# Kernel optimization log

Measured on AMD Instinct MI355X. Metric: run time of the kernel, lower is better.

Reference implementation:

```python
import jax, jax.numpy as jnp
import numpy as np

D_MODEL = 1024
NUM_HEADS = 16
HEAD_DIM = D_MODEL // NUM_HEADS

def _trunc_normal(key, shape, std):
    # truncated normal in [-3*std, 3*std]
    return jax.random.truncated_normal(key, -3.0, 3.0, shape, dtype=jnp.float32) * std

def setup_inputs() -> dict:
    key = jax.random.key(0)
    kx, kq, kk, kv, ko = jax.random.split(key, 5)
    std = np.sqrt(2.0 / (D_MODEL + D_MODEL))
    return {
        "in_features": jax.random.normal(kx, (4, 2048, D_MODEL), dtype=jnp.float32),
        "weight_q": _trunc_normal(kq, (D_MODEL, D_MODEL), std),
        "weight_k": _trunc_normal(kk, (D_MODEL, D_MODEL), std),
        "weight_v": _trunc_normal(kv, (D_MODEL, D_MODEL), std),
        "weight_o": _trunc_normal(ko, (D_MODEL, D_MODEL), std),
    }

def reference(in_features, weight_q, weight_k, weight_v, weight_o):
    in_dtype = in_features.dtype
    x = in_features.astype(jnp.float32)
    B, S, _ = x.shape
    # projections: x @ W.T (matches torch matmul(x, weight.T))
    Q = x @ weight_q.T
    K = x @ weight_k.T
    V = x @ weight_v.T
    # [B, H, S, hd]
    Q = Q.reshape(B, S, NUM_HEADS, HEAD_DIM).transpose(0, 2, 1, 3)
    K = K.reshape(B, S, NUM_HEADS, HEAD_DIM).transpose(0, 2, 1, 3)
    V = V.reshape(B, S, NUM_HEADS, HEAD_DIM).transpose(0, 2, 1, 3)
    scores = jnp.einsum('bhqd,bhkd->bhqk', Q, K) / jnp.sqrt(jnp.float32(HEAD_DIM))
    causal = jnp.tril(jnp.ones((S, S), dtype=bool))  # [S, S]
    scores = jnp.where(causal, scores, -jnp.inf)
    attn = jax.nn.softmax(scores, axis=-1)
    out = jnp.einsum('bhqk,bhkd->bhqd', attn, V)  # [B, H, S, hd]
    out = out.transpose(0, 2, 1, 3).reshape(B, S, D_MODEL)
    out = out @ weight_o.T
    return out.astype(in_dtype)
```

## Files before the change

kernel.cpp:

```cpp
#include <hip/hip_runtime.h>
#include <stdint.h>
#include <math.h>

#define B_SZ 4
#define S_LEN 2048
#define NH 16
#define HD 64
#define DM 1024
#define M_ROWS (B_SZ * S_LEN)
#define NQ 16

typedef __bf16 bf16x8 __attribute__((ext_vector_type(8)));
typedef __bf16 bf16x4 __attribute__((ext_vector_type(4)));
typedef float f32x4 __attribute__((ext_vector_type(4)));
typedef unsigned int u32x2 __attribute__((ext_vector_type(2)));

typedef __attribute__((address_space(3))) void lds_t;
typedef __attribute__((address_space(1))) const void gbl_t;

__device__ __forceinline__ unsigned cvtpk_bf16(float a, float b) {
  unsigned r;
  asm("v_cvt_pk_bf16_f32 %0, %1, %2" : "=v"(r) : "v"(a), "v"(b));
  return r;
}

__global__ void cvt_f32_bf16(const float* __restrict__ in,
                             __bf16* __restrict__ out, int n4) {
  int i = blockIdx.x * blockDim.x + threadIdx.x;
  int stride = gridDim.x * blockDim.x;
  for (; i < n4; i += stride) {
    f32x4 v = reinterpret_cast<const f32x4*>(in)[i];
    bf16x4 o;
    o[0] = (__bf16)v[0]; o[1] = (__bf16)v[1];
    o[2] = (__bf16)v[2]; o[3] = (__bf16)v[3];
    reinterpret_cast<bf16x4*>(out)[i] = o;
  }
}

__global__ void cvt_weights(const float* __restrict__ wq, const float* __restrict__ wk,
                            const float* __restrict__ wv, const float* __restrict__ wo,
                            __bf16* __restrict__ dst) {
  const int N4 = DM * DM / 4;
  int i = blockIdx.x * blockDim.x + threadIdx.x;
  int stride = gridDim.x * blockDim.x;
  for (; i < 4 * N4; i += stride) {
    int sel = i >> 18;
    const float* src = (sel == 0) ? wq : (sel == 1) ? wk : (sel == 2) ? wv : wo;
    f32x4 v = reinterpret_cast<const f32x4*>(src)[i & (N4 - 1)];
    bf16x4 o;
    o[0] = (__bf16)v[0]; o[1] = (__bf16)v[1];
    o[2] = (__bf16)v[2]; o[3] = (__bf16)v[3];
    reinterpret_cast<bf16x4*>(dst)[i] = o;
  }
}

template <int MODE>
__global__ __launch_bounds__(256, 2) void gemm64(
    const unsigned short* __restrict__ A, const unsigned short* __restrict__ BT,
    __bf16* __restrict__ Qb, __bf16* __restrict__ Kb, __bf16* __restrict__ Vt,
    float* __restrict__ Out, int NX) {
  __shared__ __align__(16) unsigned short As[128 * 64];
  __shared__ __align__(16) unsigned short Bs[128 * 64];

  const int t = threadIdx.x, lane = t & 63, w = t >> 6;
  const int wm = w >> 1, wn = w & 1;
  const int g = lane >> 4, c = lane & 15;

  const int nwg = (int)gridDim.x;
  const int cpx = nwg >> 3;
  const int bid = (int)blockIdx.x;
  const int wg = (bid & 7) * cpx + (bid >> 3);
  const int bx = wg % NX, by = wg / NX;
  const int tm0 = by * 128, tn0 = bx * 128;
  const int K = DM;

  const int srow = t >> 3;
  const int scolb = (t & 7) << 4;
  const int ssw = scolb ^ ((srow & 7) << 4);
  const uint8_t* gA0 = (const uint8_t*)A + ((size_t)(tm0 + srow) * K) * 2 + ssw;
  const uint8_t* gB0 = (const uint8_t*)BT + ((size_t)(tn0 + srow) * K) * 2 + ssw;
  uint8_t* lA0 = (uint8_t*)As + t * 16;
  uint8_t* lB0 = (uint8_t*)Bs + t * 16;
  const int kxor = (c & 7) << 4;

  f32x4 acc[4][4] = {};

  for (int k0 = 0; k0 < K; k0 += 64) {
#pragma unroll
    for (int q = 0; q < 4; ++q) {
      __builtin_amdgcn_global_load_lds((gbl_t*)(gA0 + ((size_t)q * 32 * K + k0) * 2),
                                       (lds_t*)(lA0 + q * 4096), 16, 0, 0);
      __builtin_amdgcn_global_load_lds((gbl_t*)(gB0 + ((size_t)q * 32 * K + k0) * 2),
                                       (lds_t*)(lB0 + q * 4096), 16, 0, 0);
    }
    __syncthreads();

#pragma unroll
    for (int ks = 0; ks < 2; ++ks) {
      bf16x8 af[4], bfm[4];
#pragma unroll
      for (int mb = 0; mb < 4; ++mb)
        af[mb] = *reinterpret_cast<const bf16x8*>(
            (const uint8_t*)As + (wm * 64 + mb * 16 + c) * 128 + ((ks * 64 + g * 16) ^ kxor));
#pragma unroll
      for (int nb = 0; nb < 4; ++nb)
        bfm[nb] = *reinterpret_cast<const bf16x8*>(
            (const uint8_t*)Bs + (wn * 64 + nb * 16 + c) * 128 + ((ks * 64 + g * 16) ^ kxor));
#pragma unroll
      for (int mb = 0; mb < 4; ++mb)
#pragma unroll
        for (int nb = 0; nb < 4; ++nb)
          acc[mb][nb] = __builtin_amdgcn_mfma_f32_16x16x32_bf16(af[mb], bfm[nb], acc[mb][nb], 0, 0, 0);
    }
    __syncthreads();
  }

  const int rm0 = tm0 + wm * 64;
  const int cn0 = tn0 + wn * 64;
  const int sel = tn0 >> 10;
#pragma unroll
  for (int mb = 0; mb < 4; ++mb) {
#pragma unroll
    for (int nb = 0; nb < 4; ++nb) {
      f32x4 v = acc[mb][nb];
#pragma unroll
      for (int j = 0; j < 4; ++j) {
        int rm = rm0 + mb * 16 + g * 4 + j;
        int cn = cn0 + nb * 16 + c;
        float val = v[j];
        if (MODE == 0) {
          int b = rm >> 11, s = rm & 2047;
          int dmn = cn & 1023;
          int h = dmn >> 6, d = dmn & 63;
          if (sel == 0) {
            Qb[(((size_t)(b * NH + h) * S_LEN + s) << 6) + d] = (__bf16)(val * 0.125f);
          } else if (sel == 1) {
            Kb[(((size_t)(b * NH + h) * S_LEN + s) << 6) + d] = (__bf16)val;
          } else {
            Vt[((size_t)(b * NH + h) * HD + d) * S_LEN + s] = (__bf16)val;
          }
        } else {
          Out[(size_t)rm * DM + cn] = val;
        }
      }
    }
  }
}

template <int SPLIT>
__global__ __launch_bounds__(256, 3) void attn_kernel(
    const unsigned short* __restrict__ Qb, const unsigned short* __restrict__ Kb,
    const unsigned short* __restrict__ Vt, __bf16* __restrict__ Aout,
    __bf16* __restrict__ AP, float* __restrict__ Lp) {
  __shared__ __align__(16) unsigned short KVs[2][8192];
  __shared__ __align__(16) unsigned short Ps[4][32 * 72];

  const int t = threadIdx.x, lane = t & 63, w = t >> 6;
  const int g = lane >> 4, c = lane & 15;
  const int bh = blockIdx.y;
  const int qx = (NQ - 1) - (int)blockIdx.x / SPLIT;
  const int sp = (int)blockIdx.x % SPLIT;
  const int b = bh >> 4, h = bh & 15;
  const int q0 = qx * 128 + w * 32;

  const unsigned short* Qp = Qb + (size_t)bh * S_LEN * HD;
  const uint8_t* Kg8 = (const uint8_t*)(Kb + (size_t)bh * S_LEN * HD);
  const uint8_t* Vg8 = (const uint8_t*)(Vt + (size_t)bh * HD * S_LEN);

  const int sr = t >> 3;
  const int scb = ((t & 7) << 4) ^ ((sr & 7) << 4);
  const uint8_t* Kst = Kg8 + (size_t)sr * 128 + scb;
  const uint8_t* Vst = Vg8 + (size_t)sr * (S_LEN * 2) + scb;
  uint8_t* Ls = (uint8_t*)&KVs[0][0];

#define STAGE(buf, kvb_) do {                                                  \
    uint8_t* kd = Ls + (buf) * 16384 + t * 16;                                 \
    const uint8_t* kg = Kst + (size_t)(kvb_) * 128;                            \
    const uint8_t* vg = Vst + (size_t)(kvb_) * 2;                              \
    __builtin_amdgcn_global_load_lds((gbl_t*)kg, (lds_t*)kd, 16, 0, 0);        \
    __builtin_amdgcn_global_load_lds((gbl_t*)(kg + 32 * 128),                  \
                                     (lds_t*)(kd + 4096), 16, 0, 0);           \
    __builtin_amdgcn_global_load_lds((gbl_t*)vg, (lds_t*)(kd + 8192), 16, 0, 0);\
    __builtin_amdgcn_global_load_lds((gbl_t*)(vg + (size_t)32 * S_LEN * 2),    \
                                     (lds_t*)(kd + 12288), 16, 0, 0);          \
  } while (0)

  bf16x8 qf[2][2];
#pragma unroll
  for (int mb = 0; mb < 2; ++mb)
#pragma unroll
    for (int ks = 0; ks < 2; ++ks)
      qf[mb][ks] = *reinterpret_cast<const bf16x8*>(
          Qp + (size_t)(q0 + mb * 16 + c) * HD + ks * 32 + g * 8);

  bf16x8 onesf;
#pragma unroll
  for (int i = 0; i < 8; ++i) onesf[i] = (__bf16)1.0f;

  f32x4 oacc[2][4] = {};
  f32x4 lacc[2] = {};

  const int kxor = (c & 7) << 4;
  const int n_total = 2 * qx + 2;
  const int chunk = (n_total + SPLIT - 1) / SPLIT;
  int t0 = sp * chunk; if (t0 > n_total) t0 = n_total;
  int t1 = t0 + chunk; if (t1 > n_total) t1 = n_total;
  const int nblk_w = (q0 >> 6) + 1;

  const int st0 = (t0 < n_total) ? t0 : (n_total - 1);
  STAGE(0, st0 * 64);
  __syncthreads();

  __bf16* psw = (__bf16*)&Ps[w][0];
  const int qr = q0 + c;

  for (int kb = t0; kb < t1; ++kb) {
    const int cur = (kb - t0) & 1;
    if (kb + 1 < t1) STAGE(cur ^ 1, (kb + 1) * 64);

    if (kb < nblk_w) {
      const int kvb = kb * 64;
      const uint8_t* KL = Ls + cur * 16384;
      const uint8_t* VL = KL + 8192;

      f32x4 sacc[2][4] = {};
      __builtin_amdgcn_s_setprio(1);
#pragma unroll
      for (int ks = 0; ks < 2; ++ks) {
#pragma unroll
        for (int nb = 0; nb < 4; ++nb) {
          bf16x8 kf = *reinterpret_cast<const bf16x8*>(
              KL + (nb * 16 + c) * 128 + ((ks * 64 + g * 16) ^ kxor));
          sacc[0][nb] = __builtin_amdgcn_mfma_f32_16x16x32_bf16(kf, qf[0][ks], sacc[0][nb], 0, 0, 0);
          sacc[1][nb] = __builtin_amdgcn_mfma_f32_16x16x32_bf16(kf, qf[1][ks], sacc[1][nb], 0, 0, 0);
        }
      }
      __builtin_amdgcn_s_setprio(0);

      if (kb == nblk_w - 1) {
#pragma unroll
        for (int mb = 0; mb < 2; ++mb) {
          const int qrm = qr + mb * 16;
#pragma unroll
          for (int nb = 0; nb < 4; ++nb) {
            const int key0 = kvb + nb * 16 + g * 4;
            float p0 = (key0 + 0 <= qrm) ? __expf(sacc[mb][nb][0]) : 0.f;
            float p1 = (key0 + 1 <= qrm) ? __expf(sacc[mb][nb][1]) : 0.f;
            float p2 = (key0 + 2 <= qrm) ? __expf(sacc[mb][nb][2]) : 0.f;
            float p3 = (key0 + 3 <= qrm) ? __expf(sacc[mb][nb][3]) : 0.f;
            u32x2 pk = {cvtpk_bf16(p0, p1), cvtpk_bf16(p2, p3)};
            *reinterpret_cast<u32x2*>(psw + (mb * 16 + c) * 72 + nb * 16 + g * 4) = pk;
          }
        }
      } else {
#pragma unroll
        for (int mb = 0; mb < 2; ++mb)
#pragma unroll
          for (int nb = 0; nb < 4; ++nb) {
            float p0 = __expf(sacc[mb][nb][0]);
            float p1 = __expf(sacc[mb][nb][1]);
            float p2 = __expf(sacc[mb][nb][2]);
            float p3 = __expf(sacc[mb][nb][3]);
            u32x2 pk = {cvtpk_bf16(p0, p1), cvtpk_bf16(p2, p3)};
            *reinterpret_cast<u32x2*>(psw + (mb * 16 + c) * 72 + nb * 16 + g * 4) = pk;
          }
      }

      bf16x8 pf0_0 = *reinterpret_cast<const bf16x8*>(psw + (c) * 72 + g * 8);
      bf16x8 pf0_1 = *reinterpret_cast<const bf16x8*>(psw + (c) * 72 + 32 + g * 8);
      bf16x8 pf1_0 = *reinterpret_cast<const bf16x8*>(psw + (16 + c) * 72 + g * 8);
      bf16x8 pf1_1 = *reinterpret_cast<const bf16x8*>(psw + (16 + c) * 72 + 32 + g * 8);

      __builtin_amdgcn_s_setprio(1);
      lacc[0] = __builtin_amdgcn_mfma_f32_16x16x32_bf16(pf0_0, onesf, lacc[0], 0, 0, 0);
      lacc[0] = __builtin_amdgcn_mfma_f32_16x16x32_bf16(pf0_1, onesf, lacc[0], 0, 0, 0);
      lacc[1] = __builtin_amdgcn_mfma_f32_16x16x32_bf16(pf1_0, onesf, lacc[1], 0, 0, 0);
      lacc[1] = __builtin_amdgcn_mfma_f32_16x16x32_bf16(pf1_1, onesf, lacc[1], 0, 0, 0);

#pragma unroll
      for (int db = 0; db < 4; ++db) {
        bf16x8 vf0 = *reinterpret_cast<const bf16x8*>(
            VL + (db * 16 + c) * 128 + ((g * 16) ^ kxor));
        bf16x8 vf1 = *reinterpret_cast<const bf16x8*>(
            VL + (db * 16 + c) * 128 + ((64 + g * 16) ^ kxor));
        oacc[0][db] = __builtin_amdgcn_mfma_f32_16x16x32_bf16(pf0_0, vf0, oacc[0][db], 0, 0, 0);
        oacc[0][db] = __builtin_amdgcn_mfma_f32_16x16x32_bf16(pf0_1, vf1, oacc[0][db], 0, 0, 0);
        oacc[1][db] = __builtin_amdgcn_mfma_f32_16x16x32_bf16(pf1_0, vf0, oacc[1][db], 0, 0, 0);
        oacc[1][db] = __builtin_amdgcn_mfma_f32_16x16x32_bf16(pf1_1, vf1, oacc[1][db], 0, 0, 0);
      }
      __builtin_amdgcn_s_setprio(0);
    }
    __syncthreads();
  }
#undef STAGE

  if (SPLIT == 1) {
    float rl[2][4];
#pragma unroll
    for (int mb = 0; mb < 2; ++mb)
#pragma unroll
      for (int j = 0; j < 4; ++j) rl[mb][j] = 1.0f / lacc[mb][j];
#pragma unroll
    for (int mb = 0; mb < 2; ++mb)
#pragma unroll
      for (int db = 0; db < 4; ++db)
#pragma unroll
        for (int j = 0; j < 4; ++j) {
          float o = oacc[mb][db][j] * rl[mb][j];
          int s = q0 + mb * 16 + g * 4 + j;
          int d = db * 16 + c;
          Aout[(size_t)(b * S_LEN + s) * DM + h * HD + d] = (__bf16)o;
        }
  } else {
    __bf16* APs = AP + (size_t)(sp * (B_SZ * NH) + bh) * S_LEN * HD;
    float* Lps = Lp + (size_t)(sp * (B_SZ * NH) + bh) * S_LEN;
#pragma unroll
    for (int mb = 0; mb < 2; ++mb) {
#pragma unroll
      for (int db = 0; db < 4; ++db)
#pragma unroll
        for (int j = 0; j < 4; ++j) {
          int q = q0 + mb * 16 + g * 4 + j;
          APs[(size_t)q * HD + db * 16 + c] = (__bf16)oacc[mb][db][j];
        }
      if (c == 0) {
#pragma unroll
        for (int j = 0; j < 4; ++j)
          Lps[q0 + mb * 16 + g * 4 + j] = lacc[mb][j];
      }
    }
  }
}

__global__ void attn_combine4(const __bf16* __restrict__ AP, const float* __restrict__ Lp,
                              __bf16* __restrict__ Aout) {
  const int NIT = B_SZ * NH * S_LEN * (HD / 8);
  int i = blockIdx.x * blockDim.x + threadIdx.x;
  int stride = gridDim.x * blockDim.x;
  const size_t SOFF = (size_t)(B_SZ * NH) * S_LEN * HD;
  const size_t LOFF = (size_t)(B_SZ * NH) * S_LEN;
  for (; i < NIT; i += stride) {
    int d8 = i & 7;
    int q = (i >> 3) & (S_LEN - 1);
    int bh = i >> 14;
    size_t base = ((size_t)bh * S_LEN + q) * HD + d8 * 8;
    size_t lbase = (size_t)bh * S_LEN + q;
    float l = Lp[lbase] + Lp[LOFF + lbase] + Lp[2 * LOFF + lbase] + Lp[3 * LOFF + lbase];
    float rl = 1.0f / l;
    bf16x8 a0 = *reinterpret_cast<const bf16x8*>(AP + base);
    bf16x8 a1 = *reinterpret_cast<const bf16x8*>(AP + SOFF + base);
    bf16x8 a2 = *reinterpret_cast<const bf16x8*>(AP + 2 * SOFF + base);
    bf16x8 a3 = *reinterpret_cast<const bf16x8*>(AP + 3 * SOFF + base);
    int b = bh >> 4, h = bh & 15;
    bf16x8 o;
#pragma unroll
    for (int k = 0; k < 8; ++k)
      o[k] = (__bf16)((((float)a0[k] + (float)a1[k]) + ((float)a2[k] + (float)a3[k])) * rl);
    *reinterpret_cast<bf16x8*>(Aout + ((size_t)(b * S_LEN + q)) * DM + h * HD + d8 * 8) = o;
  }
}

extern "C" void kernel_launch(void* const* d_in, const int* in_sizes, int n_in,
                              void* d_out, int out_size, void* d_ws, size_t ws_size,
                              hipStream_t stream) {
  const float* x = (const float*)d_in[0];
  const float* wq = (const float*)d_in[1];
  const float* wk = (const float*)d_in[2];
  const float* wv = (const float*)d_in[3];
  const float* wo = (const float*)d_in[4];
  float* out = (float*)d_out;

  uint8_t* ws = (uint8_t*)d_ws;
  const size_t MB = 1024 * 1024;
  unsigned short* xb   = (unsigned short*)(ws);
  unsigned short* wcat = (unsigned short*)(ws + 16 * MB);
  unsigned short* wob  = (unsigned short*)(ws + 22 * MB);
  unsigned short* Qb   = (unsigned short*)(ws + 24 * MB);
  unsigned short* Kb   = (unsigned short*)(ws + 40 * MB);
  unsigned short* Vt   = (unsigned short*)(ws + 56 * MB);
  __bf16* AP           = (__bf16*)(ws + 72 * MB);
  float* Lp            = (float*)(ws + 16 * MB);

  {
    int n4x = (M_ROWS * DM) / 4;
    int blk = (n4x + 255) / 256; if (blk > 2048) blk = 2048;
    cvt_f32_bf16<<<blk, 256, 0, stream>>>(x, (__bf16*)xb, n4x);
    cvt_weights<<<1024, 256, 0, stream>>>(wq, wk, wv, wo, (__bf16*)wcat);
  }

  gemm64<0><<<dim3((3 * DM / 128) * (M_ROWS / 128)), 256, 0, stream>>>(
      xb, wcat, (__bf16*)Qb, (__bf16*)Kb, (__bf16*)Vt, nullptr, 3 * DM / 128);

  __bf16* Aout = (__bf16*)xb;
  if (ws_size >= (size_t)136 * MB) {
    attn_kernel<4><<<dim3(NQ * 4, B_SZ * NH), 256, 0, stream>>>(
        Qb, Kb, Vt, Aout, AP, Lp);
    attn_combine4<<<2048, 256, 0, stream>>>(AP, Lp, Aout);
  } else {
    attn_kernel<1><<<dim3(NQ, B_SZ * NH), 256, 0, stream>>>(
        Qb, Kb, Vt, Aout, nullptr, nullptr);
  }

  gemm64<1><<<dim3((DM / 128) * (M_ROWS / 128)), 256, 0, stream>>>(
      xb, wob, nullptr, nullptr, nullptr, out, DM / 128);
}
```

Baseline: 204.5 us.

## Use 256x128 tile QKV GEMM with 8 waves and phased prefetch pipeline

```diff
diff --git a/kernel.cpp b/kernel.cpp
--- a/kernel.cpp
+++ b/kernel.cpp
@@ -54,17 +54,144 @@
   }
 }
 
-template <int MODE>
-__global__ __launch_bounds__(256, 2) void gemm64(
+__global__ __launch_bounds__(512, 2) void gemm256_qkv(
     const unsigned short* __restrict__ A, const unsigned short* __restrict__ BT,
-    __bf16* __restrict__ Qb, __bf16* __restrict__ Kb, __bf16* __restrict__ Vt,
-    float* __restrict__ Out, int NX) {
+    __bf16* __restrict__ Qb, __bf16* __restrict__ Kb, __bf16* __restrict__ Vt) {
+  __shared__ __align__(16) uint8_t L[2][49152];
+
+  const int t = threadIdx.x, lane = t & 63;
+  const int wid = t >> 6;
+  const int wm = wid >> 1, wn = wid & 1;
+  const int g = lane >> 4, c = lane & 15;
+
+  const int bid = (int)blockIdx.x;
+  const int wg = (bid & 7) * 96 + (bid >> 3);
+  const int bx = wg % 24, by = wg / 24;
+  const int tm0 = by * 256, tn0 = bx * 128;
+  const int K = DM;
+
+  const int u0 = t >> 3;
+  const int colswz = ((t & 7) << 4) ^ ((u0 & 7) << 4);
+  const uint8_t* Ag = (const uint8_t*)A;
+  const uint8_t* Bg = (const uint8_t*)BT;
+
+  const int arow0 = (u0 >> 5) * 64 + (u0 & 31);
+#define STAGE_A(buf_, h_, kb_) do {                                            \
+    const uint8_t* s0 = Ag + ((size_t)(tm0 + arow0 + (h_) * 32) * K) * 2 +     \
+                        (kb_) * 128 + colswz;                                  \
+    uint8_t* d = &L[buf_][0] + (h_) * 16384 + t * 16;                          \
+    __builtin_amdgcn_global_load_lds((gbl_t*)s0, (lds_t*)d, 16, 0, 0);         \
+    __builtin_amdgcn_global_load_lds((gbl_t*)(s0 + (size_t)128 * K * 2),       \
+                                     (lds_t*)(d + 8192), 16, 0, 0);            \
+  } while (0)
+#define STAGE_B(buf_, h_, kb_) do {                                            \
+    const uint8_t* s0 = Bg + ((size_t)(tn0 + arow0 + (h_) * 32) * K) * 2 +     \
+                        (kb_) * 128 + colswz;                                  \
+    uint8_t* d = &L[buf_][0] + 32768 + (h_) * 8192 + t * 16;                   \
+    __builtin_amdgcn_global_load_lds((gbl_t*)s0, (lds_t*)d, 16, 0, 0);         \
+  } while (0)
+
+  const int kxor = (c & 7) << 4;
+  f32x4 acc[4][4] = {};
+
+  STAGE_A(0, 0, 0); STAGE_A(0, 1, 0);
+  STAGE_B(0, 0, 0); STAGE_B(0, 1, 0);
+  asm volatile("s_waitcnt vmcnt(0)" ::: "memory");
+  asm volatile("s_barrier" ::: "memory");
+
+#define PHASE(buf_, MH, NH, WAITSTR, ISSUE) do {                               \
+    const uint8_t* Ab = &L[buf_][0];                                           \
+    const uint8_t* Bb = &L[buf_][0] + 32768;                                   \
+    bf16x8 af[2][2], bf[2][2];                                                 \
+    _Pragma("unroll") for (int i = 0; i < 2; ++i) {                            \
+      const int mf = MH * 2 + i;                                               \
+      const int r = (mf >> 1) * 16384 + (wm * 32 + (mf & 1) * 16 + c) * 128;   \
+      af[i][0] = *reinterpret_cast<const bf16x8*>(Ab + r + ((g * 16) ^ kxor)); \
+      af[i][1] = *reinterpret_cast<const bf16x8*>(Ab + r + ((64 + g * 16) ^ kxor)); \
+    }                                                                          \
+    _Pragma("unroll") for (int j = 0; j < 2; ++j) {                            \
+      const int nf = NH * 2 + j;                                               \
+      const int r = (nf >> 1) * 8192 + (wn * 32 + (nf & 1) * 16 + c) * 128;    \
+      bf[j][0] = *reinterpret_cast<const bf16x8*>(Bb + r + ((g * 16) ^ kxor)); \
+      bf[j][1] = *reinterpret_cast<const bf16x8*>(Bb + r + ((64 + g * 16) ^ kxor)); \
+    }                                                                          \
+    WAITSTR;                                                                   \
+    ISSUE;                                                                     \
+    asm volatile("s_barrier" ::: "memory");                                    \
+    __builtin_amdgcn_s_setprio(1);                                            \
+    _Pragma("unroll") for (int i = 0; i < 2; ++i)                              \
+      _Pragma("unroll") for (int j = 0; j < 2; ++j) {                          \
+        acc[MH * 2 + i][NH * 2 + j] = __builtin_amdgcn_mfma_f32_16x16x32_bf16( \
+            af[i][0], bf[j][0], acc[MH * 2 + i][NH * 2 + j], 0, 0, 0);         \
+        acc[MH * 2 + i][NH * 2 + j] = __builtin_amdgcn_mfma_f32_16x16x32_bf16( \
+            af[i][1], bf[j][1], acc[MH * 2 + i][NH * 2 + j], 0, 0, 0);         \
+      }                                                                        \
+    __builtin_amdgcn_s_setprio(0);                                            \
+    asm volatile("s_barrier" ::: "memory");                                    \
+  } while (0)
+
+  const int NT = K / 64;
+  for (int kb = 0; kb < NT; ++kb) {
+    const int cur = kb & 1;
+    const int nxt = cur ^ 1;
+    const int kn = (kb + 1 < NT) ? (kb + 1) : (NT - 1);
+    const int kc = kn * 128;
+
+    PHASE(cur, 0, 0,
+          asm volatile("s_waitcnt vmcnt(2)" ::: "memory"),
+          STAGE_A(nxt, 0, kn));
+    PHASE(cur, 0, 1,
+          asm volatile("s_waitcnt vmcnt(2)" ::: "memory"),
+          do { STAGE_B(nxt, 0, kn); STAGE_B(nxt, 1, kn); } while (0));
+    PHASE(cur, 1, 0, (void)0, STAGE_A(nxt, 1, kn));
+    PHASE(cur, 1, 1,
+          asm volatile("s_waitcnt vmcnt(3)" ::: "memory"),
+          (void)0);
+    (void)kc;
+  }
+  asm volatile("s_waitcnt vmcnt(0)" ::: "memory");
+#undef PHASE
+#undef STAGE_A
+#undef STAGE_B
+
+  const int rm0 = tm0 + wm * 64;
+  const int cn0 = tn0 + wn * 64;
+  const int sel = tn0 >> 10;
+#pragma unroll
+  for (int mf = 0; mf < 4; ++mf) {
+#pragma unroll
+    for (int nf = 0; nf < 4; ++nf) {
+      f32x4 v = acc[mf][nf];
+#pragma unroll
+      for (int j = 0; j < 4; ++j) {
+        int rm = rm0 + mf * 16 + g * 4 + j;
+        int cn = cn0 + nf * 16 + c;
+        int b = rm >> 11, s = rm & 2047;
+        int dmn = cn & 1023;
+        int h = dmn >> 6, d = dmn & 63;
+        float val = v[j];
+        if (sel == 0) {
+          Qb[(((size_t)(b * NH + h) * S_LEN + s) << 6) + d] = (__bf16)(val * 0.125f);
+        } else if (sel == 1) {
+          Kb[(((size_t)(b * NH + h) * S_LEN + s) << 6) + d] = (__bf16)val;
+        } else {
+          Vt[((size_t)(b * NH + h) * HD + d) * S_LEN + s] = (__bf16)val;
+        }
+      }
+    }
+  }
+}
+
+__global__ __launch_bounds__(256, 2) void gemm64_o(
+    const unsigned short* __restrict__ A, const unsigned short* __restrict__ BT,
+    float* __restrict__ Out) {
   __shared__ __align__(16) unsigned short As[128 * 64];
   __shared__ __align__(16) unsigned short Bs[128 * 64];
 
   const int t = threadIdx.x, lane = t & 63, w = t >> 6;
   const int wm = w >> 1, wn = w & 1;
   const int g = lane >> 4, c = lane & 15;
+  const int NX = DM / 128;
 
   const int nwg = (int)gridDim.x;
   const int cpx = nwg >> 3;
@@ -117,9 +244,8 @@
 
   const int rm0 = tm0 + wm * 64;
   const int cn0 = tn0 + wn * 64;
-  const int sel = tn0 >> 10;
-#pragma unroll
-  for (int mb = 0; mb < 4; ++mb) {
+#pragma unroll
+  for (int mb = 0; mb < 4; ++mb)
 #pragma unroll
     for (int nb = 0; nb < 4; ++nb) {
       f32x4 v = acc[mb][nb];
@@ -127,24 +253,9 @@
       for (int j = 0; j < 4; ++j) {
         int rm = rm0 + mb * 16 + g * 4 + j;
         int cn = cn0 + nb * 16 + c;
-        float val = v[j];
-        if (MODE == 0) {
-          int b = rm >> 11, s = rm & 2047;
-          int dmn = cn & 1023;
-          int h = dmn >> 6, d = dmn & 63;
-          if (sel == 0) {
-            Qb[(((size_t)(b * NH + h) * S_LEN + s) << 6) + d] = (__bf16)(val * 0.125f);
-          } else if (sel == 1) {
-            Kb[(((size_t)(b * NH + h) * S_LEN + s) << 6) + d] = (__bf16)val;
-          } else {
-            Vt[((size_t)(b * NH + h) * HD + d) * S_LEN + s] = (__bf16)val;
-          }
-        } else {
-          Out[(size_t)rm * DM + cn] = val;
-        }
+        Out[(size_t)rm * DM + cn] = v[j];
       }
     }
-  }
 }
 
 template <int SPLIT>
@@ -388,8 +499,8 @@
     cvt_weights<<<1024, 256, 0, stream>>>(wq, wk, wv, wo, (__bf16*)wcat);
   }
 
-  gemm64<0><<<dim3((3 * DM / 128) * (M_ROWS / 128)), 256, 0, stream>>>(
-      xb, wcat, (__bf16*)Qb, (__bf16*)Kb, (__bf16*)Vt, nullptr, 3 * DM / 128);
+  gemm256_qkv<<<dim3(768), 512, 0, stream>>>(
+      xb, wcat, (__bf16*)Qb, (__bf16*)Kb, (__bf16*)Vt);
 
   __bf16* Aout = (__bf16*)xb;
   if (ws_size >= (size_t)136 * MB) {
@@ -401,6 +512,5 @@
         Qb, Kb, Vt, Aout, nullptr, nullptr);
   }
 
-  gemm64<1><<<dim3((DM / 128) * (M_ROWS / 128)), 256, 0, stream>>>(
-      xb, wob, nullptr, nullptr, nullptr, out, DM / 128);
-}
+  gemm64_o<<<dim3((DM / 128) * (M_ROWS / 128)), 256, 0, stream>>>(xb, wob, out);
+}
```

Result: slower. 210.8 us (+3.1%).

## Double-buffer GEMM LDS tiles, raise MFMA priority, merge conversion kernels

Applied to the files above, without the earlier changes.

```diff
diff --git a/kernel.cpp b/kernel.cpp
--- a/kernel.cpp
+++ b/kernel.cpp
@@ -24,33 +24,33 @@
   return r;
 }
 
-__global__ void cvt_f32_bf16(const float* __restrict__ in,
-                             __bf16* __restrict__ out, int n4) {
+__global__ void cvt_all(const float* __restrict__ x,
+                        const float* __restrict__ wq, const float* __restrict__ wk,
+                        const float* __restrict__ wv, const float* __restrict__ wo,
+                        __bf16* __restrict__ xb, __bf16* __restrict__ wdst) {
+  const int NX4 = M_ROWS * DM / 4;
+  const int NW4 = DM * DM / 4;
+  const int TOT = NX4 + 4 * NW4;
   int i = blockIdx.x * blockDim.x + threadIdx.x;
   int stride = gridDim.x * blockDim.x;
-  for (; i < n4; i += stride) {
-    f32x4 v = reinterpret_cast<const f32x4*>(in)[i];
+  for (; i < TOT; i += stride) {
+    const float* src;
+    __bf16* dst;
+    int idx;
+    if (i < NX4) {
+      src = x; dst = xb; idx = i;
+    } else {
+      int j = i - NX4;
+      int sel = j >> 18;
+      src = (sel == 0) ? wq : (sel == 1) ? wk : (sel == 2) ? wv : wo;
+      dst = wdst + (size_t)sel * DM * DM;
+      idx = j & (NW4 - 1);
+    }
+    f32x4 v = reinterpret_cast<const f32x4*>(src)[idx];
     bf16x4 o;
     o[0] = (__bf16)v[0]; o[1] = (__bf16)v[1];
     o[2] = (__bf16)v[2]; o[3] = (__bf16)v[3];
-    reinterpret_cast<bf16x4*>(out)[i] = o;
-  }
-}
-
-__global__ void cvt_weights(const float* __restrict__ wq, const float* __restrict__ wk,
-                            const float* __restrict__ wv, const float* __restrict__ wo,
-                            __bf16* __restrict__ dst) {
-  const int N4 = DM * DM / 4;
-  int i = blockIdx.x * blockDim.x + threadIdx.x;
-  int stride = gridDim.x * blockDim.x;
-  for (; i < 4 * N4; i += stride) {
-    int sel = i >> 18;
-    const float* src = (sel == 0) ? wq : (sel == 1) ? wk : (sel == 2) ? wv : wo;
-    f32x4 v = reinterpret_cast<const f32x4*>(src)[i & (N4 - 1)];
-    bf16x4 o;
-    o[0] = (__bf16)v[0]; o[1] = (__bf16)v[1];
-    o[2] = (__bf16)v[2]; o[3] = (__bf16)v[3];
-    reinterpret_cast<bf16x4*>(dst)[i] = o;
+    reinterpret_cast<bf16x4*>(dst)[idx] = o;
   }
 }
 
@@ -59,8 +59,8 @@
     const unsigned short* __restrict__ A, const unsigned short* __restrict__ BT,
     __bf16* __restrict__ Qb, __bf16* __restrict__ Kb, __bf16* __restrict__ Vt,
     float* __restrict__ Out, int NX) {
-  __shared__ __align__(16) unsigned short As[128 * 64];
-  __shared__ __align__(16) unsigned short Bs[128 * 64];
+  __shared__ __align__(16) unsigned short As[2][128 * 64];
+  __shared__ __align__(16) unsigned short Bs[2][128 * 64];
 
   const int t = threadIdx.x, lane = t & 63, w = t >> 6;
   const int wm = w >> 1, wn = w & 1;
@@ -79,41 +79,53 @@
   const int ssw = scolb ^ ((srow & 7) << 4);
   const uint8_t* gA0 = (const uint8_t*)A + ((size_t)(tm0 + srow) * K) * 2 + ssw;
   const uint8_t* gB0 = (const uint8_t*)BT + ((size_t)(tn0 + srow) * K) * 2 + ssw;
-  uint8_t* lA0 = (uint8_t*)As + t * 16;
-  uint8_t* lB0 = (uint8_t*)Bs + t * 16;
   const int kxor = (c & 7) << 4;
 
+#define STAGE(buf_, k0_) do {                                                  \
+    uint8_t* lA = (uint8_t*)&As[buf_][0] + t * 16;                             \
+    uint8_t* lB = (uint8_t*)&Bs[buf_][0] + t * 16;                             \
+    _Pragma("unroll") for (int q = 0; q < 4; ++q) {                            \
+      __builtin_amdgcn_global_load_lds(                                        \
+          (gbl_t*)(gA0 + ((size_t)q * 32 * K + (k0_)) * 2),                    \
+          (lds_t*)(lA + q * 4096), 16, 0, 0);                                  \
+      __builtin_amdgcn_global_load_lds(                                        \
+          (gbl_t*)(gB0 + ((size_t)q * 32 * K + (k0_)) * 2),                    \
+          (lds_t*)(lB + q * 4096), 16, 0, 0);                                  \
+    }                                                                          \
+  } while (0)
+
   f32x4 acc[4][4] = {};
 
-  for (int k0 = 0; k0 < K; k0 += 64) {
-#pragma unroll
-    for (int q = 0; q < 4; ++q) {
-      __builtin_amdgcn_global_load_lds((gbl_t*)(gA0 + ((size_t)q * 32 * K + k0) * 2),
-                                       (lds_t*)(lA0 + q * 4096), 16, 0, 0);
-      __builtin_amdgcn_global_load_lds((gbl_t*)(gB0 + ((size_t)q * 32 * K + k0) * 2),
-                                       (lds_t*)(lB0 + q * 4096), 16, 0, 0);
+  STAGE(0, 0);
+  __syncthreads();
+
+  const int NT = K / 64;
+  for (int kt = 0; kt < NT; ++kt) {
+    const int cur = kt & 1;
+    if (kt + 1 < NT) STAGE(cur ^ 1, (kt + 1) * 64);
+
+#pragma unroll
+    for (int ks = 0; ks < 2; ++ks) {
+      bf16x8 af[4], bfm[4];
+#pragma unroll
+      for (int mb = 0; mb < 4; ++mb)
+        af[mb] = *reinterpret_cast<const bf16x8*>(
+            (const uint8_t*)&As[cur][0] + (wm * 64 + mb * 16 + c) * 128 + ((ks * 64 + g * 16) ^ kxor));
+#pragma unroll
+      for (int nb = 0; nb < 4; ++nb)
+        bfm[nb] = *reinterpret_cast<const bf16x8*>(
+            (const uint8_t*)&Bs[cur][0] + (wn * 64 + nb * 16 + c) * 128 + ((ks * 64 + g * 16) ^ kxor));
+      __builtin_amdgcn_s_setprio(1);
+#pragma unroll
+      for (int mb = 0; mb < 4; ++mb)
+#pragma unroll
+        for (int nb = 0; nb < 4; ++nb)
+          acc[mb][nb] = __builtin_amdgcn_mfma_f32_16x16x32_bf16(af[mb], bfm[nb], acc[mb][nb], 0, 0, 0);
+      __builtin_amdgcn_s_setprio(0);
     }
     __syncthreads();
-
-#pragma unroll
-    for (int ks = 0; ks < 2; ++ks) {
-      bf16x8 af[4], bfm[4];
-#pragma unroll
-      for (int mb = 0; mb < 4; ++mb)
-        af[mb] = *reinterpret_cast<const bf16x8*>(
-            (const uint8_t*)As + (wm * 64 + mb * 16 + c) * 128 + ((ks * 64 + g * 16) ^ kxor));
-#pragma unroll
-      for (int nb = 0; nb < 4; ++nb)
-        bfm[nb] = *reinterpret_cast<const bf16x8*>(
-            (const uint8_t*)Bs + (wn * 64 + nb * 16 + c) * 128 + ((ks * 64 + g * 16) ^ kxor));
-#pragma unroll
-      for (int mb = 0; mb < 4; ++mb)
-#pragma unroll
-        for (int nb = 0; nb < 4; ++nb)
-          acc[mb][nb] = __builtin_amdgcn_mfma_f32_16x16x32_bf16(af[mb], bfm[nb], acc[mb][nb], 0, 0, 0);
-    }
-    __syncthreads();
-  }
+  }
+#undef STAGE
 
   const int rm0 = tm0 + wm * 64;
   const int cn0 = tn0 + wn * 64;
@@ -381,12 +393,7 @@
   __bf16* AP           = (__bf16*)(ws + 72 * MB);
   float* Lp            = (float*)(ws + 16 * MB);
 
-  {
-    int n4x = (M_ROWS * DM) / 4;
-    int blk = (n4x + 255) / 256; if (blk > 2048) blk = 2048;
-    cvt_f32_bf16<<<blk, 256, 0, stream>>>(x, (__bf16*)xb, n4x);
-    cvt_weights<<<1024, 256, 0, stream>>>(wq, wk, wv, wo, (__bf16*)wcat);
-  }
+  cvt_all<<<2048, 256, 0, stream>>>(x, wq, wk, wv, wo, (__bf16*)xb, (__bf16*)wcat);
 
   gemm64<0><<<dim3((3 * DM / 128) * (M_ROWS / 128)), 256, 0, stream>>>(
       xb, wcat, (__bf16*)Qb, (__bf16*)Kb, (__bf16*)Vt, nullptr, 3 * DM / 128);
```

New measurement: 203.0 us. No clear change (-0.7%).
